# Performance work log

Hardware: AMD Instinct MI355X
Metric: run time of the kernel (lower is better)

## Reference

```python
import jax, jax.numpy as jnp
import numpy as np

EMBED_DIM = 768
NUM_HEADS = 12
HEAD_DIM = EMBED_DIM // NUM_HEADS


def setup_inputs() -> dict:
    key = jax.random.key(0)
    k1, k2, k3, k4, k5 = jax.random.split(key, 5)
    B, S, D = 2, 4096, EMBED_DIM
    scale = 1.0 / np.sqrt(D)
    return {
        "x": jax.random.normal(k1, (B, S, D), dtype=jnp.float32),
        "Wqkv": jax.random.normal(k2, (D, 3 * D), dtype=jnp.float32) * scale,
        "bqkv": jax.random.normal(k3, (3 * D,), dtype=jnp.float32) * 0.02,
        "Wout": jax.random.normal(k4, (D, D), dtype=jnp.float32) * scale,
        "bout": jax.random.normal(k5, (D,), dtype=jnp.float32) * 0.02,
    }


def reference(x, Wqkv, bqkv, Wout, bout):
    B, S, D = x.shape
    H, Hd = NUM_HEADS, HEAD_DIM
    # fused QKV projection: [B,S,3D]
    qkv = x @ Wqkv + bqkv
    q, k, v = jnp.split(qkv, 3, axis=-1)
    # [B,S,D] -> [B,H,S,Hd]
    q = q.reshape(B, S, H, Hd).transpose(0, 2, 1, 3)
    k = k.reshape(B, S, H, Hd).transpose(0, 2, 1, 3)
    v = v.reshape(B, S, H, Hd).transpose(0, 2, 1, 3)
    # causal SDPA (dropout_p = 0)
    scores = jnp.einsum("bhsd,bhtd->bhst", q, k) / jnp.sqrt(jnp.asarray(Hd, x.dtype))
    causal = jnp.tril(jnp.ones((S, S), dtype=bool))  # [S,S]
    scores = jnp.where(causal[None, None], scores, jnp.finfo(x.dtype).min)
    attn = jax.nn.softmax(scores, axis=-1)
    y = jnp.einsum("bhst,bhtd->bhsd", attn, v)  # [B,H,S,Hd]
    y = y.transpose(0, 2, 1, 3).reshape(B, S, D)
    return y @ Wout + bout
```

## Files before the change

### kernel.cpp

```cpp
#include <hip/hip_runtime.h>

#define S_LEN 4096
#define NH 12
#define HD 64
#define DMODEL 768
#define BATCH 2
#define MTOT (BATCH * S_LEN)

typedef __bf16 bf16x8 __attribute__((ext_vector_type(8)));
typedef __bf16 bf16x4 __attribute__((ext_vector_type(4)));
typedef float f32x4 __attribute__((ext_vector_type(4)));
typedef float f32x8 __attribute__((ext_vector_type(8)));

#define SM_SCALE_LOG2E 0.18033688f
#define SLAB_STRIDE 33792

__device__ __forceinline__ f32x4 f32x4_zero() {
  f32x4 z = {0.f, 0.f, 0.f, 0.f};
  return z;
}

__device__ __forceinline__ void async16(const __bf16* g, void* l) {
  __builtin_amdgcn_global_load_lds(
      (const __attribute__((address_space(1))) void*)g,
      (__attribute__((address_space(3))) void*)l, 16, 0, 0);
}

__global__ __launch_bounds__(256) void prep_all(const float* __restrict__ x,
                                                const float* __restrict__ Wqkv,
                                                const float* __restrict__ Wout,
                                                __bf16* __restrict__ xb,
                                                __bf16* __restrict__ Wqkv_t,
                                                __bf16* __restrict__ Wout_t) {
  __shared__ __bf16 t[64][72];
  const int bid = blockIdx.x;
  if (bid < 3072) {
    int i = bid * 256 + threadIdx.x;
    f32x8 a = ((const f32x8*)x)[i];
    bf16x8 o;
#pragma unroll
    for (int j = 0; j < 8; ++j) o[j] = (__bf16)a[j];
    ((bf16x8*)xb)[i] = o;
    return;
  }
  const float* in;
  __bf16* out;
  int N, v;
  if (bid < 3504) {
    in = Wqkv;
    out = Wqkv_t;
    N = 3 * DMODEL;
    v = bid - 3072;
  } else {
    in = Wout;
    out = Wout_t;
    N = DMODEL;
    v = bid - 3504;
  }
  int kb = (v % 12) * 64, nb = (v / 12) * 64;
  int c = threadIdx.x & 63, r0 = threadIdx.x >> 6;
#pragma unroll
  for (int i = 0; i < 16; ++i) {
    int r = r0 * 16 + i;
    t[c][r] = (__bf16)in[(size_t)(kb + r) * N + nb + c];
  }
  __syncthreads();
#pragma unroll
  for (int i = 0; i < 16; ++i) {
    int r = r0 * 16 + i;
    out[(size_t)(nb + r) * DMODEL + kb + c] = t[r][c];
  }
}

__device__ __forceinline__ void gemm128_bt(const __bf16* __restrict__ A,
                                           const __bf16* __restrict__ Bt,
                                           int m0, int n0, int K,
                                           __bf16* Alds, __bf16* Blds,
                                           f32x4 acc[4][4]) {
  const int tid = threadIdx.x;
  const int l = tid & 63, w = tid >> 6;
  const int wr = w >> 1, wc = w & 1;
  const int g = l >> 4, ln = l & 15;

  const int rr = tid >> 3;
  const int sx = (tid & 7) ^ (rr & 7);
  const __bf16* As = A + (size_t)(m0 + rr) * K + sx * 8;
  const __bf16* Bs = Bt + (size_t)(n0 + rr) * K + sx * 8;
  char* Ad = (char*)Alds + (w << 10);
  char* Bd = (char*)Blds + (w << 10);

  for (int k0 = 0; k0 < K; k0 += 64) {
#pragma unroll
    for (int i = 0; i < 4; ++i) {
      async16(As + (size_t)(i * 32) * K + k0, Ad + i * 4096);
      async16(Bs + (size_t)(i * 32) * K + k0, Bd + i * 4096);
    }
    __syncthreads();
#pragma unroll
    for (int kk = 0; kk < 2; ++kk) {
      bf16x8 af[4], bfr[4];
#pragma unroll
      for (int mi = 0; mi < 4; ++mi) {
        int row = wr * 64 + mi * 16 + ln;
        af[mi] = *(const bf16x8*)(Alds + row * 64 + ((((kk << 2) + g) ^ (row & 7)) << 3));
      }
#pragma unroll
      for (int ni = 0; ni < 4; ++ni) {
        int row = wc * 64 + ni * 16 + ln;
        bfr[ni] = *(const bf16x8*)(Blds + row * 64 + ((((kk << 2) + g) ^ (row & 7)) << 3));
      }
#pragma unroll
      for (int mi = 0; mi < 4; ++mi)
#pragma unroll
        for (int ni = 0; ni < 4; ++ni)
          acc[mi][ni] =
              __builtin_amdgcn_mfma_f32_16x16x32_bf16(af[mi], bfr[ni], acc[mi][ni], 0, 0, 0);
    }
    __syncthreads();
  }
}

__global__ __launch_bounds__(256) void gemm_qkv(const __bf16* __restrict__ xb,
                                                const __bf16* __restrict__ Wt,
                                                const float* __restrict__ bqkv,
                                                __bf16* __restrict__ Qo,
                                                __bf16* __restrict__ Ko,
                                                __bf16* __restrict__ Vto) {
  __shared__ __bf16 Alds[128 * 64];
  __shared__ __bf16 Blds[128 * 64];
  int bm = blockIdx.x & 63, bn = blockIdx.x >> 6;
  int m0 = bm * 128, n0 = bn * 128;
  f32x4 acc[4][4];
#pragma unroll
  for (int i = 0; i < 4; ++i)
#pragma unroll
    for (int j = 0; j < 4; ++j) acc[i][j] = f32x4_zero();
  gemm128_bt(xb, Wt, m0, n0, DMODEL, Alds, Blds, acc);

  const int l = threadIdx.x & 63, w = threadIdx.x >> 6;
  const int wr = w >> 1, wc = w & 1, g = l >> 4, ln = l & 15;
#pragma unroll
  for (int ni = 0; ni < 4; ++ni) {
    int ncol = n0 + wc * 64 + ni * 16 + ln;
    int which = ncol / DMODEL;
    int dd = ncol - which * DMODEL;
    int h = dd >> 6, hd = dd & 63;
    float bias = bqkv[ncol];
    if (which == 2) {
#pragma unroll
      for (int mi = 0; mi < 4; ++mi)
#pragma unroll
        for (int r = 0; r < 4; ++r) {
          int mrow = m0 + wr * 64 + mi * 16 + 4 * g + r;
          int b = mrow >> 12, s = mrow & (S_LEN - 1);
          float v = acc[mi][ni][r] + bias;
          Vto[(((size_t)(b * NH + h) * HD) + hd) * S_LEN + s] = (__bf16)v;
        }
    } else {
      __bf16* op = (which == 0) ? Qo : Ko;
      const float scl = (which == 0) ? SM_SCALE_LOG2E : 1.0f;
#pragma unroll
      for (int mi = 0; mi < 4; ++mi)
#pragma unroll
        for (int r = 0; r < 4; ++r) {
          int mrow = m0 + wr * 64 + mi * 16 + 4 * g + r;
          int b = mrow >> 12, s = mrow & (S_LEN - 1);
          float v = (acc[mi][ni][r] + bias) * scl;
          op[((((size_t)b * NH + h) * S_LEN) + s) * HD + hd] = (__bf16)v;
        }
    }
  }
}

__global__ __launch_bounds__(256) void gemm_out(const __bf16* __restrict__ yb,
                                                const __bf16* __restrict__ Wt,
                                                const float* __restrict__ bout,
                                                float* __restrict__ out) {
  __shared__ __bf16 Alds[128 * 64];
  __shared__ __bf16 Blds[128 * 64];
  int bm = blockIdx.x & 63, bn = blockIdx.x >> 6;
  int m0 = bm * 128, n0 = bn * 128;
  f32x4 acc[4][4];
#pragma unroll
  for (int i = 0; i < 4; ++i)
#pragma unroll
    for (int j = 0; j < 4; ++j) acc[i][j] = f32x4_zero();
  gemm128_bt(yb, Wt, m0, n0, DMODEL, Alds, Blds, acc);

  const int l = threadIdx.x & 63, w = threadIdx.x >> 6;
  const int wr = w >> 1, wc = w & 1, g = l >> 4, ln = l & 15;
#pragma unroll
  for (int ni = 0; ni < 4; ++ni) {
    int ncol = n0 + wc * 64 + ni * 16 + ln;
    float bias = bout[ncol];
#pragma unroll
    for (int mi = 0; mi < 4; ++mi)
#pragma unroll
      for (int r = 0; r < 4; ++r) {
        int mrow = m0 + wr * 64 + mi * 16 + 4 * g + r;
        out[(size_t)mrow * DMODEL + ncol] = acc[mi][ni][r] + bias;
      }
  }
}

__global__ __launch_bounds__(1024) void attn_fwd22(const __bf16* __restrict__ Q,
                                                   const __bf16* __restrict__ K,
                                                   const __bf16* __restrict__ Vt,
                                                   __bf16* __restrict__ Y,
                                                   char* __restrict__ Po) {
  __shared__ __bf16 KVl[2][2][4096];
  __shared__ char Plb[16][2048];

  const int tid = threadIdx.x;
  const int wv = tid >> 6, l = tid & 63;
  const int g = l >> 4, ln = l & 15;
  const int bi = blockIdx.x;
  const int xcd = bi & 7, j = bi >> 3;
  const int head = xcd * 3 + (j % 3);
  const int r_ = j / 3;

  int c, part, np;
  bool split;
  if (r_ < 16) {
    c = 15 - (r_ >> 2);
    part = r_ & 3;
    np = 4;
    split = true;
  } else if (r_ < 28) {
    int q = r_ - 16;
    c = 11 - q / 3;
    part = q % 3;
    np = 3;
    split = true;
  } else if (r_ < 36) {
    int q = r_ - 28;
    c = 7 - (q >> 1);
    part = q & 1;
    np = 2;
    split = true;
  } else {
    c = 39 - r_;
    part = 0;
    np = 1;
    split = false;
  }
  const int T = 4 * c + 4;
  const int base = T / np, rem = T % np;
  const int t0 = part * base + (part < rem ? part : rem);
  const int t1 = t0 + base + (part < rem ? 1 : 0);

  const int q0 = 256 * c + 16 * wv;

  const size_t hb = (size_t)head * (S_LEN * HD);
  const __bf16* Qh = Q + hb;
  const __bf16* Kh = K + hb;
  const __bf16* Vh = Vt + hb;

  const int sw = (ln & 7) << 4;
  char* Pw = Plb[wv] + ln * 128;

  const int st = tid & 511;
  const int rr = st >> 3;
  const int ss = (st & 7) ^ (rr & 7);
  const bool isK = tid < 512;
  const size_t gL = isK ? ((size_t)rr * HD + ss * 8) : ((size_t)rr * S_LEN + ss * 8);
  const int ldso = (wv & 7) << 10;

  bf16x8 qf[2];
#pragma unroll
  for (int t = 0; t < 2; ++t)
    qf[t] = *(const bf16x8*)(Qh + (size_t)(q0 + ln) * HD + 32 * t + 8 * g);

  bf16x8 ones;
#pragma unroll
  for (int t = 0; t < 8; ++t) ones[t] = (__bf16)1.0f;

  f32x4 o[4], o5;
#pragma unroll
  for (int nt = 0; nt < 4; ++nt) o[nt] = f32x4_zero();
  o5 = f32x4_zero();

  const __bf16* kq = Kh + (size_t)t0 * 64 * HD;
  const __bf16* vq = Vh + t0 * 64;
  {
    if (isK) async16(kq + gL, (char*)&KVl[0][0][0] + ldso);
    else async16(vq + gL, (char*)&KVl[0][1][0] + ldso);
    __syncthreads();
  }
  kq += (size_t)64 * HD;
  vq += 64;

  int cur = 0;
  for (int i = t0; i < t1; ++i) {
    const bool more = (i + 1) < t1;
    if (more) {
      if (isK) async16(kq + gL, (char*)&KVl[cur ^ 1][0][0] + ldso);
      else async16(vq + gL, (char*)&KVl[cur ^ 1][1][0] + ldso);
      kq += (size_t)64 * HD;
      vq += 64;
    }

    const __bf16* Kl = &KVl[cur][0][0];
    const __bf16* Vl = &KVl[cur][1][0];
    const int rel = q0 - 64 * i;

    if (rel > -16) {
      if (rel >= 63) {
#pragma unroll
        for (int jt = 0; jt < 4; ++jt) {
          int row = 16 * jt + ln;
          bf16x8 kf0 = *(const bf16x8*)(Kl + row * 64 + ((g ^ (row & 7)) << 3));
          bf16x8 kf1 = *(const bf16x8*)(Kl + row * 64 + (((4 + g) ^ (row & 7)) << 3));
          f32x4 z = f32x4_zero();
          z = __builtin_amdgcn_mfma_f32_16x16x32_bf16(kf0, qf[0], z, 0, 0, 0);
          z = __builtin_amdgcn_mfma_f32_16x16x32_bf16(kf1, qf[1], z, 0, 0, 0);
          bf16x4 qd;
#pragma unroll
          for (int r = 0; r < 4; ++r) qd[r] = (__bf16)__builtin_exp2f(z[r]);
          *(bf16x4*)(Pw + ((32 * jt + 8 * g) ^ sw)) = qd;
        }
      } else {
        const int thr = rel + ln;
#pragma unroll
        for (int jt = 0; jt < 4; ++jt) {
          int row = 16 * jt + ln;
          bf16x8 kf0 = *(const bf16x8*)(Kl + row * 64 + ((g ^ (row & 7)) << 3));
          bf16x8 kf1 = *(const bf16x8*)(Kl + row * 64 + (((4 + g) ^ (row & 7)) << 3));
          f32x4 z = f32x4_zero();
          z = __builtin_amdgcn_mfma_f32_16x16x32_bf16(kf0, qf[0], z, 0, 0, 0);
          z = __builtin_amdgcn_mfma_f32_16x16x32_bf16(kf1, qf[1], z, 0, 0, 0);
          bf16x4 qd;
#pragma unroll
          for (int r = 0; r < 4; ++r) {
            float pv = __builtin_exp2f(z[r]);
            if (16 * jt + 4 * g + r > thr) pv = 0.f;
            qd[r] = (__bf16)pv;
          }
          *(bf16x4*)(Pw + ((32 * jt + 8 * g) ^ sw)) = qd;
        }
      }

      bf16x8 pa0 = *(const bf16x8*)(Pw + ((16 * g) ^ sw));
      bf16x8 pa1 = *(const bf16x8*)(Pw + ((64 + 16 * g) ^ sw));
      __builtin_amdgcn_s_setprio(1);
      o5 = __builtin_amdgcn_mfma_f32_16x16x32_bf16(pa0, ones, o5, 0, 0, 0);
      o5 = __builtin_amdgcn_mfma_f32_16x16x32_bf16(pa1, ones, o5, 0, 0, 0);
#pragma unroll
      for (int nt = 0; nt < 4; ++nt) {
        int row = 16 * nt + ln;
        bf16x8 vf0 = *(const bf16x8*)(Vl + row * 64 + ((g ^ (row & 7)) << 3));
        bf16x8 vf1 = *(const bf16x8*)(Vl + row * 64 + (((4 + g) ^ (row & 7)) << 3));
        o[nt] = __builtin_amdgcn_mfma_f32_16x16x32_bf16(pa0, vf0, o[nt], 0, 0, 0);
        o[nt] = __builtin_amdgcn_mfma_f32_16x16x32_bf16(pa1, vf1, o[nt], 0, 0, 0);
      }
      __builtin_amdgcn_s_setprio(0);
    }

    if (more) __syncthreads();
    cur ^= 1;
  }

  if (!split) {
    const int bb = head / NH, hh = head - bb * NH;
    __bf16* Yp = Y + ((size_t)bb * S_LEN) * DMODEL + hh * HD;
#pragma unroll
    for (int r = 0; r < 4; ++r) {
      float inv = 1.0f / o5[r];
      int qr = q0 + 4 * g + r;
#pragma unroll
      for (int nt = 0; nt < 4; ++nt)
        Yp[(size_t)qr * DMODEL + 16 * nt + ln] = (__bf16)(o[nt][r] * inv);
    }
  } else {
    int soff;
    if (c < 8) soff = (c - 4) * 2 + part;
    else if (c < 12) soff = 8 + (c - 8) * 3 + part;
    else soff = 20 + (c - 12) * 4 + part;
    char* slab = Po + ((size_t)head * 36 + soff) * SLAB_STRIDE;
#pragma unroll
    for (int r = 0; r < 4; ++r) {
      int rowL = 16 * wv + 4 * g + r;
#pragma unroll
      for (int nt = 0; nt < 4; ++nt)
        *(__bf16*)(slab + (rowL * 64 + 16 * nt + ln) * 2) = (__bf16)o[nt][r];
      if (ln == 0) *(float*)(slab + 32768 + rowL * 4) = o5[r];
    }
  }
}

__global__ __launch_bounds__(256) void attn_combine(const char* __restrict__ Po,
                                                    __bf16* __restrict__ Y) {
  const int blk = blockIdx.x;
  const int head = blk / 96, rem = blk - head * 96;
  const int cc = rem >> 3, eighth = rem & 7;
  const int c = cc + 4;
  int np, boff;
  if (c < 8) {
    np = 2;
    boff = (c - 4) * 2;
  } else if (c < 12) {
    np = 3;
    boff = 8 + (c - 8) * 3;
  } else {
    np = 4;
    boff = 20 + (c - 12) * 4;
  }
  const char* s = Po + ((size_t)head * 36 + boff) * SLAB_STRIDE;
  const int tid = threadIdx.x;
  const int row = eighth * 32 + (tid >> 3), d0 = (tid & 7) * 8;

  float acc[8] = {0.f, 0.f, 0.f, 0.f, 0.f, 0.f, 0.f, 0.f};
  float rs = 0.f;
  for (int p = 0; p < np; ++p) {
    bf16x8 a = *(const bf16x8*)(s + (size_t)p * SLAB_STRIDE + (row * 64 + d0) * 2);
#pragma unroll
    for (int j = 0; j < 8; ++j) acc[j] += (float)a[j];
    rs += *(const float*)(s + (size_t)p * SLAB_STRIDE + 32768 + row * 4);
  }
  float inv = 1.0f / rs;

  const int bb = head / NH, hh = head - bb * NH;
  __bf16* yp = Y + ((size_t)bb * S_LEN + 256 * c + row) * DMODEL + hh * HD + d0;
  bf16x8 o;
#pragma unroll
  for (int j = 0; j < 8; ++j) o[j] = (__bf16)(acc[j] * inv);
  *(bf16x8*)yp = o;
}

extern "C" void kernel_launch(void* const* d_in, const int* in_sizes, int n_in,
                              void* d_out, int out_size, void* d_ws, size_t ws_size,
                              hipStream_t stream) {
  const float* x = (const float*)d_in[0];
  const float* Wqkv = (const float*)d_in[1];
  const float* bqkv = (const float*)d_in[2];
  const float* Wout = (const float*)d_in[3];
  const float* bout = (const float*)d_in[4];
  float* out = (float*)d_out;

  char* ws = (char*)d_ws;
  size_t off = 0;
  auto take = [&](size_t bytes) {
    char* p = ws + off;
    off += bytes;
    return p;
  };
  const size_t MD2 = (size_t)MTOT * DMODEL * 2;
  __bf16* xb = (__bf16*)take(MD2);
  __bf16* Wqkv_t = (__bf16*)take((size_t)3 * DMODEL * DMODEL * 2);
  __bf16* Wout_t = (__bf16*)take((size_t)DMODEL * DMODEL * 2);
  __bf16* Qb = (__bf16*)take(MD2);
  __bf16* Kb = (__bf16*)take(MD2);
  __bf16* Vtb = (__bf16*)take(MD2);
  __bf16* Yb = (__bf16*)take(MD2);
  char* Po = take((size_t)24 * 36 * SLAB_STRIDE);

  prep_all<<<3648, 256, 0, stream>>>(x, Wqkv, Wout, xb, Wqkv_t, Wout_t);
  gemm_qkv<<<64 * (3 * DMODEL / 128), 256, 0, stream>>>(xb, Wqkv_t, bqkv, Qb, Kb, Vtb);
  attn_fwd22<<<960, 1024, 0, stream>>>(Qb, Kb, Vtb, Yb, Po);
  attn_combine<<<2304, 256, 0, stream>>>(Po, Yb);
  gemm_out<<<64 * (DMODEL / 128), 256, 0, stream>>>(Yb, Wout_t, bout, out);
}
```

Before: 182.7 us.

## Shrink attention query chunks to 160 rows with 640-thread blocks and rebalance splits

The attention kernel now processes 160-query chunks per block using 10 waves instead of 256 queries with 16 waves. The causal work split (4/3/2/1 parts per chunk), the partial-result slab layout and the combine kernel's indexing are all recomputed for 26 chunks per head. K and V tile loads are redistributed across the 640 threads, with overlapping thread ranges. The last chunk is partially inactive and is guarded. The goal is a finer, better-balanced grid with more blocks resident per CU, at the cost of more K/V reloads per query and more combine traffic.

```diff
diff --git a/kernel.cpp b/kernel.cpp
--- a/kernel.cpp
+++ b/kernel.cpp
@@ -13,7 +13,7 @@
 typedef float f32x8 __attribute__((ext_vector_type(8)));
 
 #define SM_SCALE_LOG2E 0.18033688f
-#define SLAB_STRIDE 33792
+#define SLAB_STRIDE 21120
 
 __device__ __forceinline__ f32x4 f32x4_zero() {
   f32x4 z = {0.f, 0.f, 0.f, 0.f};
@@ -203,13 +203,13 @@
   }
 }
 
-__global__ __launch_bounds__(1024) void attn_fwd22(const __bf16* __restrict__ Q,
-                                                   const __bf16* __restrict__ K,
-                                                   const __bf16* __restrict__ Vt,
-                                                   __bf16* __restrict__ Y,
-                                                   char* __restrict__ Po) {
+__global__ __launch_bounds__(640) void attn_fwd24(const __bf16* __restrict__ Q,
+                                                  const __bf16* __restrict__ K,
+                                                  const __bf16* __restrict__ Vt,
+                                                  __bf16* __restrict__ Y,
+                                                  char* __restrict__ Po) {
   __shared__ __bf16 KVl[2][2][4096];
-  __shared__ char Plb[16][2048];
+  __shared__ char Plb[10][2048];
 
   const int tid = threadIdx.x;
   const int wv = tid >> 6, l = tid & 63;
@@ -220,36 +220,35 @@
   const int r_ = j / 3;
 
   int c, part, np;
-  bool split;
-  if (r_ < 16) {
-    c = 15 - (r_ >> 2);
+  if (r_ < 28) {
+    c = 25 - (r_ >> 2);
     part = r_ & 3;
     np = 4;
-    split = true;
-  } else if (r_ < 28) {
-    int q = r_ - 16;
-    c = 11 - q / 3;
+  } else if (r_ < 49) {
+    int q = r_ - 28;
+    c = 18 - q / 3;
     part = q % 3;
     np = 3;
-    split = true;
-  } else if (r_ < 36) {
-    int q = r_ - 28;
-    c = 7 - (q >> 1);
+  } else if (r_ < 61) {
+    int q = r_ - 49;
+    c = 11 - (q >> 1);
     part = q & 1;
     np = 2;
-    split = true;
   } else {
-    c = 39 - r_;
+    c = 66 - r_;
     part = 0;
     np = 1;
-    split = false;
-  }
-  const int T = 4 * c + 4;
+  }
+  const bool split = np > 1;
+  int T = (160 * (c + 1) + 63) / 64;
+  if (T > 64) T = 64;
   const int base = T / np, rem = T % np;
   const int t0 = part * base + (part < rem ? part : rem);
   const int t1 = t0 + base + (part < rem ? 1 : 0);
 
-  const int q0 = 256 * c + 16 * wv;
+  const int q0 = 160 * c + 16 * wv;
+  const bool active = q0 < S_LEN;
+  const int q0s = active ? q0 : 0;
 
   const size_t hb = (size_t)head * (S_LEN * HD);
   const __bf16* Qh = Q + hb;
@@ -259,17 +258,20 @@
   const int sw = (ln & 7) << 4;
   char* Pw = Plb[wv] + ln * 128;
 
-  const int st = tid & 511;
-  const int rr = st >> 3;
-  const int ss = (st & 7) ^ (rr & 7);
-  const bool isK = tid < 512;
-  const size_t gL = isK ? ((size_t)rr * HD + ss * 8) : ((size_t)rr * S_LEN + ss * 8);
-  const int ldso = (wv & 7) << 10;
+  const bool doK = tid < 512;
+  const bool doV = tid >= 128;
+  const int kr = tid >> 3, ks2 = (tid & 7) ^ (kr & 7);
+  const int vt = tid - 128;
+  const int vr = vt >> 3, vs2 = (vt & 7) ^ (vr & 7);
+  const size_t kL = (size_t)kr * HD + ks2 * 8;
+  const size_t vL = (size_t)vr * S_LEN + vs2 * 8;
+  const int ldsoK = wv << 10;
+  const int ldsoV = (wv - 2) << 10;
 
   bf16x8 qf[2];
 #pragma unroll
   for (int t = 0; t < 2; ++t)
-    qf[t] = *(const bf16x8*)(Qh + (size_t)(q0 + ln) * HD + 32 * t + 8 * g);
+    qf[t] = *(const bf16x8*)(Qh + (size_t)(q0s + ln) * HD + 32 * t + 8 * g);
 
   bf16x8 ones;
 #pragma unroll
@@ -283,8 +285,8 @@
   const __bf16* kq = Kh + (size_t)t0 * 64 * HD;
   const __bf16* vq = Vh + t0 * 64;
   {
-    if (isK) async16(kq + gL, (char*)&KVl[0][0][0] + ldso);
-    else async16(vq + gL, (char*)&KVl[0][1][0] + ldso);
+    if (doK) async16(kq + kL, (char*)&KVl[0][0][0] + ldsoK);
+    if (doV) async16(vq + vL, (char*)&KVl[0][1][0] + ldsoV);
     __syncthreads();
   }
   kq += (size_t)64 * HD;
@@ -294,8 +296,8 @@
   for (int i = t0; i < t1; ++i) {
     const bool more = (i + 1) < t1;
     if (more) {
-      if (isK) async16(kq + gL, (char*)&KVl[cur ^ 1][0][0] + ldso);
-      else async16(vq + gL, (char*)&KVl[cur ^ 1][1][0] + ldso);
+      if (doK) async16(kq + kL, (char*)&KVl[cur ^ 1][0][0] + ldsoK);
+      if (doV) async16(vq + vL, (char*)&KVl[cur ^ 1][1][0] + ldsoV);
       kq += (size_t)64 * HD;
       vq += 64;
     }
@@ -304,7 +306,7 @@
     const __bf16* Vl = &KVl[cur][1][0];
     const int rel = q0 - 64 * i;
 
-    if (rel > -16) {
+    if (active && rel > -16) {
       if (rel >= 63) {
 #pragma unroll
         for (int jt = 0; jt < 4; ++jt) {
@@ -360,30 +362,32 @@
     cur ^= 1;
   }
 
-  if (!split) {
-    const int bb = head / NH, hh = head - bb * NH;
-    __bf16* Yp = Y + ((size_t)bb * S_LEN) * DMODEL + hh * HD;
-#pragma unroll
-    for (int r = 0; r < 4; ++r) {
-      float inv = 1.0f / o5[r];
-      int qr = q0 + 4 * g + r;
-#pragma unroll
-      for (int nt = 0; nt < 4; ++nt)
-        Yp[(size_t)qr * DMODEL + 16 * nt + ln] = (__bf16)(o[nt][r] * inv);
-    }
-  } else {
-    int soff;
-    if (c < 8) soff = (c - 4) * 2 + part;
-    else if (c < 12) soff = 8 + (c - 8) * 3 + part;
-    else soff = 20 + (c - 12) * 4 + part;
-    char* slab = Po + ((size_t)head * 36 + soff) * SLAB_STRIDE;
-#pragma unroll
-    for (int r = 0; r < 4; ++r) {
-      int rowL = 16 * wv + 4 * g + r;
-#pragma unroll
-      for (int nt = 0; nt < 4; ++nt)
-        *(__bf16*)(slab + (rowL * 64 + 16 * nt + ln) * 2) = (__bf16)o[nt][r];
-      if (ln == 0) *(float*)(slab + 32768 + rowL * 4) = o5[r];
+  if (active) {
+    if (!split) {
+      const int bb = head / NH, hh = head - bb * NH;
+      __bf16* Yp = Y + ((size_t)bb * S_LEN) * DMODEL + hh * HD;
+#pragma unroll
+      for (int r = 0; r < 4; ++r) {
+        float inv = 1.0f / o5[r];
+        int qr = q0 + 4 * g + r;
+#pragma unroll
+        for (int nt = 0; nt < 4; ++nt)
+          Yp[(size_t)qr * DMODEL + 16 * nt + ln] = (__bf16)(o[nt][r] * inv);
+      }
+    } else {
+      int pref;
+      if (c < 12) pref = (c - 6) * 2;
+      else if (c < 19) pref = 12 + (c - 12) * 3;
+      else pref = 33 + (c - 19) * 4;
+      char* slab = Po + ((size_t)head * 61 + pref + part) * SLAB_STRIDE;
+#pragma unroll
+      for (int r = 0; r < 4; ++r) {
+        int rowL = 16 * wv + 4 * g + r;
+#pragma unroll
+        for (int nt = 0; nt < 4; ++nt)
+          *(__bf16*)(slab + (rowL * 64 + 16 * nt + ln) * 2) = (__bf16)o[nt][r];
+        if (ln == 0) *(float*)(slab + 20480 + rowL * 4) = o5[r];
+      }
     }
   }
 }
@@ -391,23 +395,29 @@
 __global__ __launch_bounds__(256) void attn_combine(const char* __restrict__ Po,
                                                     __bf16* __restrict__ Y) {
   const int blk = blockIdx.x;
-  const int head = blk / 96, rem = blk - head * 96;
-  const int cc = rem >> 3, eighth = rem & 7;
-  const int c = cc + 4;
-  int np, boff;
-  if (c < 8) {
+  const int head = blk / 98, rem = blk - head * 98;
+  int c, seg;
+  if (rem < 95) {
+    c = rem / 5 + 6;
+    seg = rem % 5;
+  } else {
+    c = 25;
+    seg = rem - 95;
+  }
+  int np, pref;
+  if (c < 12) {
     np = 2;
-    boff = (c - 4) * 2;
-  } else if (c < 12) {
+    pref = (c - 6) * 2;
+  } else if (c < 19) {
     np = 3;
-    boff = 8 + (c - 8) * 3;
+    pref = 12 + (c - 12) * 3;
   } else {
     np = 4;
-    boff = 20 + (c - 12) * 4;
-  }
-  const char* s = Po + ((size_t)head * 36 + boff) * SLAB_STRIDE;
+    pref = 33 + (c - 19) * 4;
+  }
+  const char* s = Po + ((size_t)head * 61 + pref) * SLAB_STRIDE;
   const int tid = threadIdx.x;
-  const int row = eighth * 32 + (tid >> 3), d0 = (tid & 7) * 8;
+  const int row = seg * 32 + (tid >> 3), d0 = (tid & 7) * 8;
 
   float acc[8] = {0.f, 0.f, 0.f, 0.f, 0.f, 0.f, 0.f, 0.f};
   float rs = 0.f;
@@ -415,12 +425,12 @@
     bf16x8 a = *(const bf16x8*)(s + (size_t)p * SLAB_STRIDE + (row * 64 + d0) * 2);
 #pragma unroll
     for (int j = 0; j < 8; ++j) acc[j] += (float)a[j];
-    rs += *(const float*)(s + (size_t)p * SLAB_STRIDE + 32768 + row * 4);
+    rs += *(const float*)(s + (size_t)p * SLAB_STRIDE + 20480 + row * 4);
   }
   float inv = 1.0f / rs;
 
   const int bb = head / NH, hh = head - bb * NH;
-  __bf16* yp = Y + ((size_t)bb * S_LEN + 256 * c + row) * DMODEL + hh * HD + d0;
+  __bf16* yp = Y + ((size_t)bb * S_LEN + 160 * c + row) * DMODEL + hh * HD + d0;
   bf16x8 o;
 #pragma unroll
   for (int j = 0; j < 8; ++j) o[j] = (__bf16)(acc[j] * inv);
@@ -452,11 +462,11 @@
   __bf16* Kb = (__bf16*)take(MD2);
   __bf16* Vtb = (__bf16*)take(MD2);
   __bf16* Yb = (__bf16*)take(MD2);
-  char* Po = take((size_t)24 * 36 * SLAB_STRIDE);
+  char* Po = take((size_t)24 * 61 * SLAB_STRIDE);
 
   prep_all<<<3648, 256, 0, stream>>>(x, Wqkv, Wout, xb, Wqkv_t, Wout_t);
   gemm_qkv<<<64 * (3 * DMODEL / 128), 256, 0, stream>>>(xb, Wqkv_t, bqkv, Qb, Kb, Vtb);
-  attn_fwd22<<<960, 1024, 0, stream>>>(Qb, Kb, Vtb, Yb, Po);
-  attn_combine<<<2304, 256, 0, stream>>>(Po, Yb);
+  attn_fwd24<<<1608, 640, 0, stream>>>(Qb, Kb, Vtb, Yb, Po);
+  attn_combine<<<2352, 256, 0, stream>>>(Po, Yb);
   gemm_out<<<64 * (DMODEL / 128), 256, 0, stream>>>(Yb, Wout_t, bout, out);
 }
```

Measured after the change: 188.1 us. 1.03x slower.
